# Performance work log

Hardware: AMD Instinct MI355X
Metric: run time of the kernel (lower is better)

The kernel has to match this reference:

```python
import jax, jax.numpy as jnp
import numpy as np


def _build_skew(coeff, gate, left, right):
    # coeff: [B, r], gate: [B], left/right: [F, r]
    scaled_left = left[None, :, :] * coeff[:, None, :]          # [B, F, r]
    base = jnp.einsum('bfr,gr->bfg', scaled_left, right)         # [B, F, F]
    skew = base - jnp.swapaxes(base, -1, -2)
    return gate[:, None, None] * skew


def setup_inputs() -> dict:
    key = jax.random.key(0)
    ks = jax.random.split(key, 10)
    B, N, F, R = 8, 4096, 512, 16
    return {
        'x': jax.random.normal(ks[0], (B, N, F), dtype=jnp.float32),
        'coeff': jax.random.normal(ks[1], (B, R), dtype=jnp.float32),
        'gate': jax.random.uniform(ks[2], (B,), dtype=jnp.float32),
        'coeff_local': jax.random.normal(ks[3], (B, R), dtype=jnp.float32),
        'gate_local': jax.random.uniform(ks[4], (B,), dtype=jnp.float32),
        'comm_scale': jax.random.uniform(ks[5], (B,), dtype=jnp.float32),
        'left': jax.random.normal(ks[6], (F, R), dtype=jnp.float32) / np.sqrt(F),
        'right': jax.random.normal(ks[7], (F, R), dtype=jnp.float32) / np.sqrt(F),
        'left_local': jax.random.normal(ks[8], (F, R), dtype=jnp.float32) / np.sqrt(F),
        'right_local': jax.random.normal(ks[9], (F, R), dtype=jnp.float32) / np.sqrt(F),
    }


def reference(x, coeff, gate, coeff_local, gate_local, comm_scale,
              left, right, left_local, right_local):
    F_dim = left.shape[0]
    global_skew = _build_skew(coeff, gate, left, right)                  # [B, F, F]
    local_skew = _build_skew(coeff_local, gate_local, left_local, right_local)
    omega = 0.5 * (global_skew + local_skew)
    commutator = local_skew @ global_skew - global_skew @ local_skew
    omega = omega + comm_scale[:, None, None] * (commutator / 12.0)
    eye = jnp.eye(F_dim, dtype=jnp.float32)[None, :, :]
    # Cayley transform: (I - 0.5*Omega)^{-1} (I + 0.5*Omega)
    transform = jnp.linalg.solve(eye - 0.5 * omega, eye + 0.5 * omega)   # [B, F, F]
    mixed = jnp.einsum('bnd,bdh->bnh', x, transform)
    return mixed.astype(x.dtype)
```

## Files before the change

kernel.cpp:

```cpp
#include <hip/hip_runtime.h>

#define B_ 8
#define N_ 4096
#define F_ 512

typedef __attribute__((ext_vector_type(8))) short bf16x8;
typedef __attribute__((ext_vector_type(4))) float f32x4;

#define XPAD 524

__device__ __forceinline__ float Sval(const float* l, const float* r,
                                      const float* ll, const float* rl,
                                      int h, int e) {
    const int m = e >> 4, c = e & 15;
    const float* p = (m == 0) ? l : (m == 1) ? r : (m == 2) ? ll : rl;
    return p[h * 16 + c];
}

__device__ __forceinline__ float qval(const float* coeff, const float* coeff_l,
                                      int b, int j) {
    if (j < 16) return 1.f;
    if (j < 32) return coeff[b * 16 + (j - 16)];
    if (j < 48) return 1.f;
    return coeff_l[b * 16 + (j - 48)];
}

__device__ __forceinline__ float lane_bcast(float v, int lane) {
    return __int_as_float(__builtin_amdgcn_readlane(__float_as_int(v), lane));
}

__device__ __forceinline__ unsigned short bf16_rn(float x) {
    unsigned u = __float_as_uint(x);
    unsigned r = u + 0x7FFFu + ((u >> 16) & 1u);
    return (unsigned short)(r >> 16);
}

__device__ __forceinline__ void bf16_split(float x, short& hi, short& lo) {
    const unsigned short h = bf16_rn(x);
    const float hf = __uint_as_float(((unsigned)h) << 16);
    const unsigned short s = bf16_rn(x - hf);
    hi = (short)h; lo = (short)s;
}

__device__ __forceinline__ float b2f(unsigned short u) {
    return __uint_as_float(((unsigned)u) << 16);
}

__global__ __launch_bounds__(256) void k_prep(const float* l, const float* r,
                                              const float* ll, const float* rl,
                                              float* GS, unsigned short* Sf) {
    __shared__ float red[4][64];
    const int i = blockIdx.x;
    const int t = threadIdx.x;
    const int j = t & 63, seg = t >> 6;

    {
        const int ht = i >> 1, eh = i & 1;
        for (int idx = t; idx < 512; idx += 256) {
            const int lx = idx >> 3, ii = idx & 7;
            const int h = ht * 16 + (lx & 15);
            const int e = eh * 32 + ((lx >> 4) & 3) * 8 + ii;
            short hh, ss;
            bf16_split(Sval(l, r, ll, rl, h, e), hh, ss);
            Sf[(i * 2 + 0) * 512 + idx] = (unsigned short)hh;
            Sf[(i * 2 + 1) * 512 + idx] = (unsigned short)ss;
        }
    }

    float acc = 0.f;
    const int h0 = seg * 128;
    for (int h = h0; h < h0 + 128; ++h)
        acc += Sval(l, r, ll, rl, h, i) * Sval(l, r, ll, rl, h, j);
    red[seg][j] = acc;
    __syncthreads();
    if (t < 64) GS[i * 64 + t] = red[0][t] + red[1][t] + red[2][t] + red[3][t];
}

__global__ __launch_bounds__(256) void k_pre(const float* coeff, const float* gate,
                                             const float* coeff_l, const float* gate_l,
                                             const float* comm, const float* GS,
                                             float* Mws, float* CPws) {
    __shared__ float GST[4096];
    __shared__ float CPs[4096];
    __shared__ float ABs[2048];
    __shared__ float u1s[32], u2s[32];

    const int b = blockIdx.x, t = threadIdx.x;
    const int tx = t & 15, ty = t >> 4;
    const float g = gate[b], gl = gate_l[b];
    const float cs = comm[b] / 12.0f;

    if (t < 32) {
        u1s[t] = (t < 16) ? g * coeff[b * 16 + t] : -g;
        u2s[t] = (t < 16) ? gl * coeff_l[b * 16 + t] : -gl;
    }
    for (int idx = t; idx < 4096; idx += 256) {
        const int i = idx & 63, e = idx >> 6;
        GST[idx] = -0.5f * qval(coeff, coeff_l, b, i) * GS[(i ^ 16) * 64 + e];
    }
    __syncthreads();

    for (int idx = t; idx < 2048; idx += 256) {
        const int which = idx >> 10;
        const int i = (idx >> 5) & 31, j = idx & 31;
        float val;
        if (which == 0) {
            const int v2i = (i < 16) ? 48 + i : 16 + i;
            const float v2sc = (i < 16) ? 1.f : coeff_l[b * 16 + (i - 16)];
            val = v2sc * u1s[j] * GS[v2i * 64 + j];
        } else {
            const int v1i = (i < 16) ? 16 + i : i - 16;
            const float v1sc = (i < 16) ? 1.f : coeff[b * 16 + (i - 16)];
            val = v1sc * u2s[j] * GS[v1i * 64 + 32 + j];
        }
        ABs[idx] = val;
    }
    __syncthreads();

    for (int idx = t; idx < 4096; idx += 256) {
        const int e = idx >> 6, j = idx & 63;
        float val = 0.f;
        if (j < 32) {
            if (e == j) val += 0.5f * u1s[j];
            if (e >= 32) val += cs * u2s[e - 32] * ABs[(e - 32) * 32 + j];
        } else {
            const int jp = j - 32;
            if (e == 32 + jp) val += 0.5f * u2s[jp];
            if (e < 32) val -= cs * u1s[e] * ABs[1024 + e * 32 + jp];
        }
        CPs[idx] = val;
        CPws[b * 4096 + idx] = val;
    }
    __syncthreads();

    {
        const int i0 = ty * 4, m0 = tx * 4;
        float acc[4][4];
#pragma unroll
        for (int i = 0; i < 4; ++i)
#pragma unroll
            for (int j = 0; j < 4; ++j) acc[i][j] = 0.f;
        for (int e = 0; e < 64; ++e) {
            const float4 av = *reinterpret_cast<const float4*>(&GST[e * 64 + i0]);
            const float4 bv = *reinterpret_cast<const float4*>(&CPs[e * 64 + m0]);
            const float a[4] = {av.x, av.y, av.z, av.w};
            const float bb[4] = {bv.x, bv.y, bv.z, bv.w};
#pragma unroll
            for (int i = 0; i < 4; ++i)
#pragma unroll
                for (int j = 0; j < 4; ++j) acc[i][j] += a[i] * bb[j];
        }
#pragma unroll
        for (int i = 0; i < 4; ++i) {
            float4 o;
            o.x = acc[i][0] + (((i0 + i) == (m0 + 0)) ? 1.f : 0.f);
            o.y = acc[i][1] + (((i0 + i) == (m0 + 1)) ? 1.f : 0.f);
            o.z = acc[i][2] + (((i0 + i) == (m0 + 2)) ? 1.f : 0.f);
            o.w = acc[i][3] + (((i0 + i) == (m0 + 3)) ? 1.f : 0.f);
            *reinterpret_cast<float4*>(&Mws[b * 4096 + (i0 + i) * 64 + m0]) = o;
        }
    }
}

#define DO64(M, K) \
    M(0, K) M(1, K) M(2, K) M(3, K) M(4, K) M(5, K) M(6, K) M(7, K) \
    M(8, K) M(9, K) M(10, K) M(11, K) M(12, K) M(13, K) M(14, K) M(15, K) \
    M(16, K) M(17, K) M(18, K) M(19, K) M(20, K) M(21, K) M(22, K) M(23, K) \
    M(24, K) M(25, K) M(26, K) M(27, K) M(28, K) M(29, K) M(30, K) M(31, K) \
    M(32, K) M(33, K) M(34, K) M(35, K) M(36, K) M(37, K) M(38, K) M(39, K) \
    M(40, K) M(41, K) M(42, K) M(43, K) M(44, K) M(45, K) M(46, K) M(47, K) \
    M(48, K) M(49, K) M(50, K) M(51, K) M(52, K) M(53, K) M(54, K) M(55, K) \
    M(56, K) M(57, K) M(58, K) M(59, K) M(60, K) M(61, K) M(62, K) M(63, K)

#define GJ_LOAD(RR, K) a[RR] = Mws[base + (RR)*64 + t];
#define GJ_STORE(RR, K) Kws[base + (RR)*64 + t] = a[RR];

#define INV_SNAP(RR, G) if (ing) Msnap[(RR) * 8 + gl] = a[RR];

#define IGU(I, G, J) \
    if ((I) != (J)) { \
        const float f_ = lane_bcast(a[(G)*8 + (I)], (G)*8 + (J)); \
        a[(G)*8 + (I)] = __builtin_fmaf(-f_, akp[J], a[(G)*8 + (I)]); \
    }

#define IGS(G, J) { \
    const float dk = lane_bcast(a[(G)*8 + (J)], (G)*8 + (J)); \
    const float pinv = 1.0f / dk; \
    a[(G)*8 + (J)] = (t == ((G)*8 + (J))) ? pinv : a[(G)*8 + (J)] * pinv; \
    akp[J] = a[(G)*8 + (J)] + ((t == ((G)*8 + (J))) ? 1.0f : 0.0f); \
    IGU(0, G, J) IGU(1, G, J) IGU(2, G, J) IGU(3, G, J) \
    IGU(4, G, J) IGU(5, G, J) IGU(6, G, J) IGU(7, G, J) }

#define TRL(RR, G) \
    if (((RR) >> 3) != (G)) { \
        const float4 m0 = *reinterpret_cast<const float4*>(&Msnap[(RR) * 8]); \
        const float4 m1 = *reinterpret_cast<const float4*>(&Msnap[(RR) * 8 + 4]); \
        a[RR] = __builtin_fmaf(-m0.x, akp[0], a[RR]); \
        a[RR] = __builtin_fmaf(-m0.y, akp[1], a[RR]); \
        a[RR] = __builtin_fmaf(-m0.z, akp[2], a[RR]); \
        a[RR] = __builtin_fmaf(-m0.w, akp[3], a[RR]); \
        a[RR] = __builtin_fmaf(-m1.x, akp[4], a[RR]); \
        a[RR] = __builtin_fmaf(-m1.y, akp[5], a[RR]); \
        a[RR] = __builtin_fmaf(-m1.z, akp[6], a[RR]); \
        a[RR] = __builtin_fmaf(-m1.w, akp[7], a[RR]); \
    }

#define MACRO_STEP(G) { \
    float akp[8]; \
    const bool ing = ((t >> 3) == (G)); \
    DO64(INV_SNAP, G) \
    IGS(G, 0) IGS(G, 1) IGS(G, 2) IGS(G, 3) \
    IGS(G, 4) IGS(G, 5) IGS(G, 6) IGS(G, 7) \
    DO64(TRL, G) }

__global__ __launch_bounds__(64, 1) void k_inv(const float* Mws, float* Kws) {
    __shared__ float Msnap[512];
    const int b = blockIdx.x, t = threadIdx.x;
    const int base = b * 4096;
    const int gl = t & 7;
    float a[64];
    DO64(GJ_LOAD, 0)
    MACRO_STEP(0) MACRO_STEP(1) MACRO_STEP(2) MACRO_STEP(3)
    MACRO_STEP(4) MACRO_STEP(5) MACRO_STEP(6) MACRO_STEP(7)
    DO64(GJ_STORE, 0)
}

__global__ __launch_bounds__(256) void k_sepost(const float* coeff, const float* coeff_l,
                                                const float* l, const float* r,
                                                const float* ll, const float* rl,
                                                const float* CPws, const float* Kws,
                                                unsigned short* SEf) {
    __shared__ float smem[12480];
    float* CPs = smem;
    float* Ks  = smem + 4224;
    float* Es  = smem + 8384;
    float* Ss  = smem;
    float* SEs = smem + 4224;

    const int b = blockIdx.y, hc = blockIdx.x, t = threadIdx.x;
    const int tx = t & 15, ty = t >> 4;

    for (int idx = t; idx < 4096; idx += 256) {
        CPs[idx] = CPws[b * 4096 + idx];
        Ks[idx] = Kws[b * 4096 + idx];
    }
    __syncthreads();

    {
        const int e0 = ty * 4, c0 = tx * 4;
        float accd[4][4];
#pragma unroll
        for (int i = 0; i < 4; ++i)
#pragma unroll
            for (int j = 0; j < 4; ++j) accd[i][j] = 0.f;
        for (int q = 0; q < 64; ++q) {
            const float4 bv = *reinterpret_cast<const float4*>(&Ks[q * 64 + c0]);
            const float bb[4] = {bv.x, bv.y, bv.z, bv.w};
            float ad[4];
#pragma unroll
            for (int i = 0; i < 4; ++i) ad[i] = CPs[(e0 + i) * 64 + q];
#pragma unroll
            for (int i = 0; i < 4; ++i)
#pragma unroll
                for (int j = 0; j < 4; ++j) accd[i][j] += ad[i] * bb[j];
        }
        float qv[4];
#pragma unroll
        for (int j = 0; j < 4; ++j) qv[j] = qval(coeff, coeff_l, b, c0 + j);
#pragma unroll
        for (int i = 0; i < 4; ++i) {
            float4 o;
            o.x = qv[0] * accd[i][0];
            o.y = qv[1] * accd[i][1];
            o.z = qv[2] * accd[i][2];
            o.w = qv[3] * accd[i][3];
            *reinterpret_cast<float4*>(&Es[(e0 + i) * 64 + (c0 ^ 16)]) = o;
        }
    }
    __syncthreads();

    for (int idx = t; idx < 4096; idx += 256) {
        const int hl_ = idx >> 6, e = idx & 63;
        Ss[hl_ * 66 + e] = Sval(l, r, ll, rl, hc * 64 + hl_, e);
    }
    __syncthreads();

    {
        const int h = t >> 2;
        const int mg = (t & 3) * 16;
        float acc[16];
#pragma unroll
        for (int q = 0; q < 16; ++q) acc[q] = 0.f;
#pragma unroll 4
        for (int e = 0; e < 64; ++e) {
            const float s = Ss[h * 66 + e];
            const float* Er = Es + e * 64 + mg;
#pragma unroll
            for (int q = 0; q < 16; ++q) acc[q] += s * Er[q];
        }
#pragma unroll
        for (int q = 0; q < 16; ++q) SEs[h * 65 + mg + q] = acc[q];
    }
    __syncthreads();

    unsigned short* outp = SEf + (size_t)b * 65536 + hc * 8192;
#pragma unroll
    for (int it = 0; it < 4; ++it) {
        const int widx0 = it * 2048 + t * 8;
        const int fl = widx0 >> 10;
        const int hl = (widx0 >> 9) & 1;
        const int lx = (widx0 >> 3) & 63;
        const int m = (fl & 3) * 16 + (lx & 15);
        const int hb = (fl >> 2) * 32 + ((lx >> 4) & 3) * 8;
        unsigned short wv[8];
#pragma unroll
        for (int i = 0; i < 8; ++i) {
            short hh, ss;
            bf16_split(SEs[(hb + i) * 65 + m], hh, ss);
            wv[i] = hl ? (unsigned short)ss : (unsigned short)hh;
        }
        uint4 pk;
        pk.x = (unsigned)wv[0] | ((unsigned)wv[1] << 16);
        pk.y = (unsigned)wv[2] | ((unsigned)wv[3] << 16);
        pk.z = (unsigned)wv[4] | ((unsigned)wv[5] << 16);
        pk.w = (unsigned)wv[6] | ((unsigned)wv[7] << 16);
        *reinterpret_cast<uint4*>(outp + widx0) = pk;
    }
}

__global__ __launch_bounds__(256, 4) void k_mix(const float* x,
                                                const unsigned short* SEf,
                                                const unsigned short* Sf,
                                                float* out) {
    __shared__ unsigned short xh[16 * XPAD];
    __shared__ unsigned short xl[16 * XPAD];
    __shared__ float Zs[16 * 68];
    const int b = blockIdx.y;
    const int r0 = blockIdx.x * 16;
    const int t = threadIdx.x;
    const int w = t >> 6;
    const int l = t & 63;
    const int lm = l & 15;
    const int lk = (l >> 4) * 8;
    const float* xb = x + (size_t)b * N_ * F_;
    float* outb = out + (size_t)b * N_ * F_;
    const unsigned short* sef = SEf + (size_t)b * 65536;

#pragma unroll 4
    for (int it = 0; it < 8; ++it) {
        const int idx = it * 256 + t;
        const int row = idx >> 7, c4 = (idx & 127) * 4;
        const float4 v = *reinterpret_cast<const float4*>(
            xb + (size_t)(r0 + row) * F_ + c4);
        ushort4 hs, ls;
        short hh, ss;
        bf16_split(v.x, hh, ss); hs.x = (unsigned short)hh; ls.x = (unsigned short)ss;
        bf16_split(v.y, hh, ss); hs.y = (unsigned short)hh; ls.y = (unsigned short)ss;
        bf16_split(v.z, hh, ss); hs.z = (unsigned short)hh; ls.z = (unsigned short)ss;
        bf16_split(v.w, hh, ss); hs.w = (unsigned short)hh; ls.w = (unsigned short)ss;
        *reinterpret_cast<ushort4*>(&xh[row * XPAD + c4]) = hs;
        *reinterpret_cast<ushort4*>(&xl[row * XPAD + c4]) = ls;
    }
    __syncthreads();

    f32x4 ahh = {0.f, 0.f, 0.f, 0.f}, alh = ahh, ahl = ahh;
    const unsigned short* xhr = xh + lm * XPAD;
    const unsigned short* xlr = xl + lm * XPAD;
#pragma unroll 4
    for (int kk = 0; kk < 16; ++kk) {
        const int k0 = kk * 32 + lk;
        const bf16x8 ah = *reinterpret_cast<const bf16x8*>(xhr + k0);
        const bf16x8 al = *reinterpret_cast<const bf16x8*>(xlr + k0);
        const int o0 = (kk * 4 + w) * 1024 + l * 8;
        const bf16x8 bh = *reinterpret_cast<const bf16x8*>(sef + o0);
        const bf16x8 bl = *reinterpret_cast<const bf16x8*>(sef + o0 + 512);
        ahh = __builtin_amdgcn_mfma_f32_16x16x32_bf16(ah, bh, ahh, 0, 0, 0);
        alh = __builtin_amdgcn_mfma_f32_16x16x32_bf16(al, bh, alh, 0, 0, 0);
        ahl = __builtin_amdgcn_mfma_f32_16x16x32_bf16(ah, bl, ahl, 0, 0, 0);
    }
#pragma unroll
    for (int r = 0; r < 4; ++r) {
        const int zr = ((l >> 4) * 4 + r) * 68 + w * 16;
        Zs[zr + lm] = ahh[r] + alh[r] + ahl[r];
    }
    __syncthreads();

    bf16x8 zh0, zl0, zh1, zl1;
    {
        const float* zrow = &Zs[lm * 68];
#pragma unroll
        for (int i = 0; i < 8; ++i) {
            short hh, ss;
            bf16_split(zrow[lk + i], hh, ss);
            zh0[i] = hh; zl0[i] = ss;
            bf16_split(zrow[32 + lk + i], hh, ss);
            zh1[i] = hh; zl1[i] = ss;
        }
    }
    const int lrow0 = (l >> 4) * 4;
    const int orow0 = r0 + lrow0;
#pragma unroll 2
    for (int j2 = 0; j2 < 8; ++j2) {
        const int ht = w * 8 + j2;
        const int h0 = ht * 16 + lm;
        f32x4 ca = {0.f, 0.f, 0.f, 0.f};
        f32x4 cb;
#pragma unroll
        for (int r = 0; r < 4; ++r) {
            const int la = (lrow0 + r) * XPAD + h0;
            cb[r] = b2f(xh[la]) + b2f(xl[la]);
        }
        const int fb = ht * 2048 + l * 8;
        const bf16x8 bh0 = *reinterpret_cast<const bf16x8*>(Sf + fb);
        const bf16x8 bl0 = *reinterpret_cast<const bf16x8*>(Sf + fb + 512);
        const bf16x8 bh1 = *reinterpret_cast<const bf16x8*>(Sf + fb + 1024);
        const bf16x8 bl1 = *reinterpret_cast<const bf16x8*>(Sf + fb + 1536);
        ca = __builtin_amdgcn_mfma_f32_16x16x32_bf16(zh0, bh0, ca, 0, 0, 0);
        ca = __builtin_amdgcn_mfma_f32_16x16x32_bf16(zl0, bh0, ca, 0, 0, 0);
        ca = __builtin_amdgcn_mfma_f32_16x16x32_bf16(zh0, bl0, ca, 0, 0, 0);
        cb = __builtin_amdgcn_mfma_f32_16x16x32_bf16(zh1, bh1, cb, 0, 0, 0);
        cb = __builtin_amdgcn_mfma_f32_16x16x32_bf16(zl1, bh1, cb, 0, 0, 0);
        cb = __builtin_amdgcn_mfma_f32_16x16x32_bf16(zh1, bl1, cb, 0, 0, 0);
#pragma unroll
        for (int r = 0; r < 4; ++r)
            outb[(size_t)(orow0 + r) * F_ + h0] = ca[r] + cb[r];
    }
}

extern "C" void kernel_launch(void* const* d_in, const int* in_sizes, int n_in,
                              void* d_out, int out_size, void* d_ws, size_t ws_size,
                              hipStream_t stream) {
    (void)in_sizes; (void)n_in; (void)out_size; (void)ws_size;
    const float* x       = (const float*)d_in[0];
    const float* coeff   = (const float*)d_in[1];
    const float* gate    = (const float*)d_in[2];
    const float* coeff_l = (const float*)d_in[3];
    const float* gate_l  = (const float*)d_in[4];
    const float* comm    = (const float*)d_in[5];
    const float* l       = (const float*)d_in[6];
    const float* r       = (const float*)d_in[7];
    const float* ll      = (const float*)d_in[8];
    const float* rl      = (const float*)d_in[9];

    char* wsb = (char*)d_ws;
    float* GS   = (float*)(wsb);
    unsigned short* SEf = (unsigned short*)(wsb + 147456);
    unsigned short* Sf  = (unsigned short*)(wsb + 1196032);
    float* Mws  = (float*)(wsb + 1327104);
    float* CPws = (float*)(wsb + 1458176);
    float* Kws  = (float*)(wsb + 1589248);
    float* out = (float*)d_out;

    k_prep<<<dim3(64), dim3(256), 0, stream>>>(l, r, ll, rl, GS, Sf);
    k_pre<<<dim3(8), dim3(256), 0, stream>>>(coeff, gate, coeff_l, gate_l, comm, GS,
                                             Mws, CPws);
    k_inv<<<dim3(8), dim3(64), 0, stream>>>(Mws, Kws);
    k_sepost<<<dim3(8, 8), dim3(256), 0, stream>>>(coeff, coeff_l, l, r, ll, rl,
                                                   CPws, Kws, SEf);
    k_mix<<<dim3(256, 8), dim3(256), 0, stream>>>(x, SEf, Sf, out);
}
```

Before: 107.3 us.

## Split 64x64 Gauss-Jordan inversion across four wavefronts per batch

The in-register block Gauss-Jordan inversion now runs on 256 threads (four wavefronts), each holding 16 rows instead of one wavefront holding all 64. For each 8-column panel, the owning wave does the pivot steps and publishes the pivot rows through LDS. The other waves read them after a barrier and all waves apply the trailing update with lane broadcasts. This targets the serial latency of the small inversion kernel, at the cost of two block barriers per panel and LDS traffic.

```diff
diff --git a/kernel.cpp b/kernel.cpp
--- a/kernel.cpp
+++ b/kernel.cpp
@@ -162,67 +162,79 @@
     }
 }
 
-#define DO64(M, K) \
-    M(0, K) M(1, K) M(2, K) M(3, K) M(4, K) M(5, K) M(6, K) M(7, K) \
-    M(8, K) M(9, K) M(10, K) M(11, K) M(12, K) M(13, K) M(14, K) M(15, K) \
-    M(16, K) M(17, K) M(18, K) M(19, K) M(20, K) M(21, K) M(22, K) M(23, K) \
-    M(24, K) M(25, K) M(26, K) M(27, K) M(28, K) M(29, K) M(30, K) M(31, K) \
-    M(32, K) M(33, K) M(34, K) M(35, K) M(36, K) M(37, K) M(38, K) M(39, K) \
-    M(40, K) M(41, K) M(42, K) M(43, K) M(44, K) M(45, K) M(46, K) M(47, K) \
-    M(48, K) M(49, K) M(50, K) M(51, K) M(52, K) M(53, K) M(54, K) M(55, K) \
-    M(56, K) M(57, K) M(58, K) M(59, K) M(60, K) M(61, K) M(62, K) M(63, K)
-
-#define GJ_LOAD(RR, K) a[RR] = Mws[base + (RR)*64 + t];
-#define GJ_STORE(RR, K) Kws[base + (RR)*64 + t] = a[RR];
-
-#define INV_SNAP(RR, G) if (ing) Msnap[(RR) * 8 + gl] = a[RR];
-
-#define IGU(I, G, J) \
+#define DO16(M) M(0) M(1) M(2) M(3) M(4) M(5) M(6) M(7) \
+                M(8) M(9) M(10) M(11) M(12) M(13) M(14) M(15)
+
+#define GJL(I) a[I] = Mws[base + (wv * 16 + (I)) * 64 + ln];
+#define GJS(I) Kws[base + (wv * 16 + (I)) * 64 + ln] = a[I];
+
+#define IP_UPD(I, BQ, J) \
     if ((I) != (J)) { \
-        const float f_ = lane_bcast(a[(G)*8 + (I)], (G)*8 + (J)); \
-        a[(G)*8 + (I)] = __builtin_fmaf(-f_, akp[J], a[(G)*8 + (I)]); \
-    }
-
-#define IGS(G, J) { \
-    const float dk = lane_bcast(a[(G)*8 + (J)], (G)*8 + (J)); \
+        const float f_ = lane_bcast(a[(BQ) + (I)], g8 + (J)); \
+        a[(BQ) + (I)] = __builtin_fmaf(-f_, akp##J, a[(BQ) + (I)]); \
+    }
+
+#define IP_STEP(BQ, J) { \
+    const float dk = lane_bcast(a[(BQ) + (J)], g8 + (J)); \
     const float pinv = 1.0f / dk; \
-    a[(G)*8 + (J)] = (t == ((G)*8 + (J))) ? pinv : a[(G)*8 + (J)] * pinv; \
-    akp[J] = a[(G)*8 + (J)] + ((t == ((G)*8 + (J))) ? 1.0f : 0.0f); \
-    IGU(0, G, J) IGU(1, G, J) IGU(2, G, J) IGU(3, G, J) \
-    IGU(4, G, J) IGU(5, G, J) IGU(6, G, J) IGU(7, G, J) }
-
-#define TRL(RR, G) \
-    if (((RR) >> 3) != (G)) { \
-        const float4 m0 = *reinterpret_cast<const float4*>(&Msnap[(RR) * 8]); \
-        const float4 m1 = *reinterpret_cast<const float4*>(&Msnap[(RR) * 8 + 4]); \
-        a[RR] = __builtin_fmaf(-m0.x, akp[0], a[RR]); \
-        a[RR] = __builtin_fmaf(-m0.y, akp[1], a[RR]); \
-        a[RR] = __builtin_fmaf(-m0.z, akp[2], a[RR]); \
-        a[RR] = __builtin_fmaf(-m0.w, akp[3], a[RR]); \
-        a[RR] = __builtin_fmaf(-m1.x, akp[4], a[RR]); \
-        a[RR] = __builtin_fmaf(-m1.y, akp[5], a[RR]); \
-        a[RR] = __builtin_fmaf(-m1.z, akp[6], a[RR]); \
-        a[RR] = __builtin_fmaf(-m1.w, akp[7], a[RR]); \
-    }
-
-#define MACRO_STEP(G) { \
-    float akp[8]; \
-    const bool ing = ((t >> 3) == (G)); \
-    DO64(INV_SNAP, G) \
-    IGS(G, 0) IGS(G, 1) IGS(G, 2) IGS(G, 3) \
-    IGS(G, 4) IGS(G, 5) IGS(G, 6) IGS(G, 7) \
-    DO64(TRL, G) }
-
-__global__ __launch_bounds__(64, 1) void k_inv(const float* Mws, float* Kws) {
-    __shared__ float Msnap[512];
+    a[(BQ) + (J)] = (ln == g8 + (J)) ? pinv : a[(BQ) + (J)] * pinv; \
+    akp##J = a[(BQ) + (J)] + ((ln == g8 + (J)) ? 1.0f : 0.0f); \
+    akp_lds[(J) * 64 + ln] = akp##J; \
+    IP_UPD(0, BQ, J) IP_UPD(1, BQ, J) IP_UPD(2, BQ, J) IP_UPD(3, BQ, J) \
+    IP_UPD(4, BQ, J) IP_UPD(5, BQ, J) IP_UPD(6, BQ, J) IP_UPD(7, BQ, J) }
+
+#define IP_ALL(BQ) \
+    IP_STEP(BQ, 0) IP_STEP(BQ, 1) IP_STEP(BQ, 2) IP_STEP(BQ, 3) \
+    IP_STEP(BQ, 4) IP_STEP(BQ, 5) IP_STEP(BQ, 6) IP_STEP(BQ, 7)
+
+#define TRAIL(I) \
+    if (((wv * 16 + (I)) >> 3) != G) { \
+        const float f0 = lane_bcast(a[I], g8 + 0); \
+        const float f1 = lane_bcast(a[I], g8 + 1); \
+        const float f2 = lane_bcast(a[I], g8 + 2); \
+        const float f3 = lane_bcast(a[I], g8 + 3); \
+        const float f4 = lane_bcast(a[I], g8 + 4); \
+        const float f5 = lane_bcast(a[I], g8 + 5); \
+        const float f6 = lane_bcast(a[I], g8 + 6); \
+        const float f7 = lane_bcast(a[I], g8 + 7); \
+        a[I] = __builtin_fmaf(-f0, akp0, a[I]); \
+        a[I] = __builtin_fmaf(-f1, akp1, a[I]); \
+        a[I] = __builtin_fmaf(-f2, akp2, a[I]); \
+        a[I] = __builtin_fmaf(-f3, akp3, a[I]); \
+        a[I] = __builtin_fmaf(-f4, akp4, a[I]); \
+        a[I] = __builtin_fmaf(-f5, akp5, a[I]); \
+        a[I] = __builtin_fmaf(-f6, akp6, a[I]); \
+        a[I] = __builtin_fmaf(-f7, akp7, a[I]); \
+    }
+
+__global__ __launch_bounds__(256, 1) void k_inv(const float* Mws, float* Kws) {
+    __shared__ float akp_lds[512];
     const int b = blockIdx.x, t = threadIdx.x;
+    const int wv = t >> 6, ln = t & 63;
     const int base = b * 4096;
-    const int gl = t & 7;
-    float a[64];
-    DO64(GJ_LOAD, 0)
-    MACRO_STEP(0) MACRO_STEP(1) MACRO_STEP(2) MACRO_STEP(3)
-    MACRO_STEP(4) MACRO_STEP(5) MACRO_STEP(6) MACRO_STEP(7)
-    DO64(GJ_STORE, 0)
+    float a[16];
+    DO16(GJL)
+    float akp0, akp1, akp2, akp3, akp4, akp5, akp6, akp7;
+    for (int G = 0; G < 8; ++G) {
+        const int g8 = G * 8;
+        __syncthreads();
+        if (wv == (G >> 1)) {
+            if ((G & 1) == 0) { IP_ALL(0) } else { IP_ALL(8) }
+        }
+        __syncthreads();
+        if (wv != (G >> 1)) {
+            akp0 = akp_lds[0 * 64 + ln];
+            akp1 = akp_lds[1 * 64 + ln];
+            akp2 = akp_lds[2 * 64 + ln];
+            akp3 = akp_lds[3 * 64 + ln];
+            akp4 = akp_lds[4 * 64 + ln];
+            akp5 = akp_lds[5 * 64 + ln];
+            akp6 = akp_lds[6 * 64 + ln];
+            akp7 = akp_lds[7 * 64 + ln];
+        }
+        DO16(TRAIL)
+    }
+    DO16(GJS)
 }
 
 __global__ __launch_bounds__(256) void k_sepost(const float* coeff, const float* coeff_l,
@@ -454,7 +466,7 @@
     k_prep<<<dim3(64), dim3(256), 0, stream>>>(l, r, ll, rl, GS, Sf);
     k_pre<<<dim3(8), dim3(256), 0, stream>>>(coeff, gate, coeff_l, gate_l, comm, GS,
                                              Mws, CPws);
-    k_inv<<<dim3(8), dim3(64), 0, stream>>>(Mws, Kws);
+    k_inv<<<dim3(8), dim3(256), 0, stream>>>(Mws, Kws);
     k_sepost<<<dim3(8, 8), dim3(256), 0, stream>>>(coeff, coeff_l, l, r, ll, rl,
                                                    CPws, Kws, SEf);
     k_mix<<<dim3(256, 8), dim3(256), 0, stream>>>(x, SEf, Sf, out);
```

Result: faster. 99.15 us (-7.6%).
